# Performance work log

Hardware: AMD Instinct MI355X
Metric: run time of the kernel (lower is better)

## Reference

```python
import jax, jax.numpy as jnp
import numpy as np

B = 64
SEG = 4096
N = B * SEG
C = 512
MID = 4 * C
EPS = 1e-5


def setup_inputs() -> dict:
    key = jax.random.key(0)
    ks = jax.random.split(key, 8)
    s_in = 1.0 / np.sqrt(C)
    s_mid = 1.0 / np.sqrt(MID)
    return {
        "x2": jax.random.normal(ks[0], (N, C), dtype=jnp.float32),
        "npoint": jnp.full((B,), SEG, dtype=jnp.int64) if jax.config.jax_enable_x64 else jnp.full((B,), SEG, dtype=jnp.int32),
        "W1a": jax.random.normal(ks[1], (C, MID), dtype=jnp.float32) * s_in,
        "g1a": jnp.ones((MID,), dtype=jnp.float32),
        "b1a": jnp.zeros((MID,), dtype=jnp.float32),
        "W2a": jax.random.normal(ks[2], (MID, C), dtype=jnp.float32) * s_mid,
        "W1b": jax.random.normal(ks[3], (C, MID), dtype=jnp.float32) * s_in,
        "g1b": jnp.ones((MID,), dtype=jnp.float32),
        "b1b": jnp.zeros((MID,), dtype=jnp.float32),
        "W2b": jax.random.normal(ks[4], (MID, C), dtype=jnp.float32) * s_mid,
    }


def _bn(h, g, b):
    # training-mode BatchNorm1d over the segment (batch) axis
    m = jnp.mean(h, axis=0)
    v = jnp.var(h, axis=0)
    return (h - m) * jax.lax.rsqrt(v + EPS) * g + b


def reference(x2, npoint, W1a, g1a, b1a, W2a, W1b, g1b, b1b, W2b):
    n = x2.shape[0]
    b = npoint.shape[0]
    # segment id for every point: seg[j] = i  iff  cumsum(npoint)[i-1] <= j < cumsum(npoint)[i]
    cum = jnp.cumsum(npoint)
    seg = jnp.searchsorted(cum, jnp.arange(n), side="right")  # [N]
    counts = npoint.astype(x2.dtype)  # [B]
    # per-segment mean  [B, C]
    mean_f = jax.ops.segment_sum(x2, seg, num_segments=b) / counts[:, None]
    # fc branch: Linear -> BN -> ReLU -> Linear -> ReLU
    ha = jax.nn.relu(_bn(mean_f @ W1a, g1a, b1a))
    out_mean = jax.nn.relu(ha @ W2a)  # [B, C]
    # fc1 branch + sigmoid
    hb = jax.nn.relu(_bn(mean_f @ W1b, g1b, b1b))
    out_w = jax.nn.sigmoid(jax.nn.relu(hb @ W2b))  # [B, C]
    # broadcast per-segment stats back to points and combine
    return out_w[seg] * x2 * 0.5 + x2 * 0.75 + out_mean[seg]
```

## Files before the change

kernel.cpp:

```cpp
#include <hip/hip_runtime.h>
#include <hip/hip_bf16.h>
#include <math.h>

#define NB    64
#define CD    512
#define CV    128
#define MIDD  2048
#define RS    32
#define EPSV  1e-5f

__device__ __forceinline__ float wave_sum64(float x) {
    #pragma unroll
    for (int o = 32; o; o >>= 1) x += __shfl_xor(x, o, 64);
    return x;
}

__global__ __launch_bounds__(128) void k_partial(const float* __restrict__ x2,
                          const int* __restrict__ npoint,
                          float* __restrict__ P) {
    int bx = blockIdx.x;
    int b  = bx >> 5;
    int rs = bx & (RS - 1);
    int start = 0;
    for (int i = 0; i < b; ++i) start += npoint[i];
    int len   = npoint[b];
    int chunk = (len + RS - 1) / RS;
    int r0 = rs * chunk;
    int r1 = min(r0 + chunk, len);
    int t = threadIdx.x;
    const float4* xv = (const float4*)x2;
    float4 acc = make_float4(0.f, 0.f, 0.f, 0.f);
    #pragma unroll 8
    for (int r = r0; r < r1; ++r) {
        float4 v = xv[(size_t)(start + r) * CV + t];
        acc.x += v.x; acc.y += v.y; acc.z += v.z; acc.w += v.w;
    }
    ((float4*)P)[(size_t)bx * CV + t] = acc;
}

__global__ __launch_bounds__(128) void k_mean(const float* __restrict__ P,
                       const int* __restrict__ npoint,
                       float* __restrict__ mean_t,
                       int* __restrict__ cum) {
    int b = blockIdx.x;
    int t = threadIdx.x;
    const float4* Pv = (const float4*)P;
    float4 acc = make_float4(0.f, 0.f, 0.f, 0.f);
    #pragma unroll
    for (int rs = 0; rs < RS; ++rs) {
        float4 v = Pv[((size_t)(b * RS + rs)) * CV + t];
        acc.x += v.x; acc.y += v.y; acc.z += v.z; acc.w += v.w;
    }
    float inv = 1.0f / (float)npoint[b];
    int c = 4 * t;
    mean_t[(size_t)(c + 0) * NB + b] = acc.x * inv;
    mean_t[(size_t)(c + 1) * NB + b] = acc.y * inv;
    mean_t[(size_t)(c + 2) * NB + b] = acc.z * inv;
    mean_t[(size_t)(c + 3) * NB + b] = acc.w * inv;
    if (t == 0) {
        int s = 0;
        for (int i = 0; i <= b; ++i) s += npoint[i];
        cum[b] = s;
    }
}

__global__ __launch_bounds__(512) void k_fc1(const float* __restrict__ mean_t,
                                             const float* __restrict__ W1a,
                                             const float* __restrict__ g1a,
                                             const float* __restrict__ b1a,
                                             const float* __restrict__ W1b,
                                             const float* __restrict__ g1b,
                                             const float* __restrict__ b1b,
                                             float* __restrict__ h_t) {
    __shared__ float red[8][64][9];
    int bx = blockIdx.x;
    int branch = bx >> 8;
    int cg = bx & 255;
    int c0 = cg * 8;
    const float* W1 = branch ? W1b : W1a;
    const float* g  = branch ? g1b : g1a;
    const float* bb = branch ? b1b : b1a;
    int t = threadIdx.x;
    int lane = t & 63;
    int w = t >> 6;
    float acc[8];
    #pragma unroll
    for (int i = 0; i < 8; ++i) acc[i] = 0.f;
    int k0 = w * 64;
    for (int k = k0; k < k0 + 64; ++k) {
        float mval = mean_t[(size_t)k * NB + lane];
        const float4* wr = (const float4*)(W1 + (size_t)k * MIDD + c0);
        float4 w0 = wr[0], w1 = wr[1];
        acc[0] += mval * w0.x; acc[1] += mval * w0.y;
        acc[2] += mval * w0.z; acc[3] += mval * w0.w;
        acc[4] += mval * w1.x; acc[5] += mval * w1.y;
        acc[6] += mval * w1.z; acc[7] += mval * w1.w;
    }
    #pragma unroll
    for (int i = 0; i < 8; ++i) red[w][lane][i] = acc[i];
    __syncthreads();
    float v = red[0][lane][w];
    #pragma unroll
    for (int ww = 1; ww < 8; ++ww) v += red[ww][lane][w];
    float s = wave_sum64(v);
    float m = s * (1.0f / 64.0f);
    float d = v - m;
    float q = wave_sum64(d * d);
    float var = q * (1.0f / 64.0f);
    float val = fmaxf(d * rsqrtf(var + EPSV) * g[c0 + w] + bb[c0 + w], 0.0f);
    h_t[((size_t)branch * MIDD + c0 + w) * NB + lane] = val;
}

__global__ __launch_bounds__(512) void k_fc2(const float* __restrict__ h_t,
                                             const float* __restrict__ W2a,
                                             const float* __restrict__ W2b,
                                             float* __restrict__ out_mean,
                                             float* __restrict__ out_w) {
    __shared__ float red[8][64][9];
    int bx = blockIdx.x;
    int branch = bx >> 6;
    int cg = bx & 63;
    int c0 = cg * 8;
    const float* W2 = branch ? W2b : W2a;
    int t = threadIdx.x;
    int lane = t & 63;
    int w = t >> 6;
    float acc[8];
    #pragma unroll
    for (int i = 0; i < 8; ++i) acc[i] = 0.f;
    int k0 = w * 256;
    for (int k = k0; k < k0 + 256; ++k) {
        float hv = h_t[((size_t)branch * MIDD + k) * NB + lane];
        const float4* wr = (const float4*)(W2 + (size_t)k * CD + c0);
        float4 w0 = wr[0], w1 = wr[1];
        acc[0] += hv * w0.x; acc[1] += hv * w0.y;
        acc[2] += hv * w0.z; acc[3] += hv * w0.w;
        acc[4] += hv * w1.x; acc[5] += hv * w1.y;
        acc[6] += hv * w1.z; acc[7] += hv * w1.w;
    }
    #pragma unroll
    for (int i = 0; i < 8; ++i) red[w][lane][i] = acc[i];
    __syncthreads();
    float v = red[0][lane][w];
    #pragma unroll
    for (int ww = 1; ww < 8; ++ww) v += red[ww][lane][w];
    float r = fmaxf(v, 0.0f);
    if (branch)
        out_w[(size_t)lane * CD + c0 + w] = 1.0f / (1.0f + expf(-r));
    else
        out_mean[(size_t)lane * CD + c0 + w] = r;
}

__global__ __launch_bounds__(256) void k_final(const float* __restrict__ x2,
                        const int* __restrict__ cum,
                        const float* __restrict__ out_mean,
                        const float* __restrict__ out_w,
                        float* __restrict__ out) {
    int t = threadIdx.x;
    int lane = t & 63;
    int w = t >> 6;
    size_t base = (size_t)blockIdx.x << 10;
    int base_row = blockIdx.x << 3;
    int row = base_row + 2 * lane + (w >> 1);
    int lo = 0, hi = NB - 1;
    while (lo < hi) {
        int mid = (lo + hi) >> 1;
        if (cum[mid] > row) hi = mid; else lo = mid + 1;
    }
    const float4* xv = (const float4*)x2;
    const float4* wv = (const float4*)out_w;
    const float4* mv = (const float4*)out_mean;
    float4* ov = (float4*)out;
    int colv = t & 127;
    float4 x0 = xv[base + t];
    float4 x1 = xv[base + 256 + t];
    float4 x2v = xv[base + 512 + t];
    float4 x3 = xv[base + 768 + t];
    float4 xs[4] = {x0, x1, x2v, x3};
    #pragma unroll
    for (int k = 0; k < 4; ++k) {
        int seg = __shfl(lo, k, 64);
        float4 x = xs[k];
        float4 ww = wv[(size_t)seg * CV + colv];
        float4 mm = mv[(size_t)seg * CV + colv];
        float4 o;
        o.x = x.x * (0.5f * ww.x + 0.75f) + mm.x;
        o.y = x.y * (0.5f * ww.y + 0.75f) + mm.y;
        o.z = x.z * (0.5f * ww.z + 0.75f) + mm.z;
        o.w = x.w * (0.5f * ww.w + 0.75f) + mm.w;
        ov[base + ((size_t)k << 8) + t] = o;
    }
}

extern "C" void kernel_launch(void* const* d_in, const int* in_sizes, int n_in,
                              void* d_out, int out_size, void* d_ws, size_t ws_size,
                              hipStream_t stream) {
    const float* x2  = (const float*)d_in[0];
    const int*   npt = (const int*)d_in[1];
    const float* W1a = (const float*)d_in[2];
    const float* g1a = (const float*)d_in[3];
    const float* b1a = (const float*)d_in[4];
    const float* W2a = (const float*)d_in[5];
    const float* W1b = (const float*)d_in[6];
    const float* g1b = (const float*)d_in[7];
    const float* b1b = (const float*)d_in[8];
    const float* W2b = (const float*)d_in[9];
    float* out = (float*)d_out;

    const int N   = in_sizes[0] / CD;
    const int NC4 = (N * CD) / 4;

    float* P      = out;
    float* mean_t = out + (size_t)NB * RS * CD;
    float* h_t    = mean_t + (size_t)NB * CD;
    int*   cum      = (int*)d_ws;
    float* out_mean = (float*)d_ws + 64;
    float* out_w    = out_mean + (size_t)NB * CD;

    k_partial<<<NB * RS, 128, 0, stream>>>(x2, npt, P);
    k_mean<<<NB, 128, 0, stream>>>(P, npt, mean_t, cum);
    k_fc1<<<2 * (MIDD / 8), 512, 0, stream>>>(mean_t, W1a, g1a, b1a, W1b, g1b, b1b, h_t);
    k_fc2<<<2 * (CD / 8), 512, 0, stream>>>(h_t, W2a, W2b, out_mean, out_w);
    k_final<<<NC4 / 1024, 256, 0, stream>>>(x2, cum, out_mean, out_w, out);
}
```

Measured before the change: 374.3 us.

## Widen final kernel with nontemporal IO, reverse block order, uniform-segment fast path

The final broadcast kernel now handles 16 rows per block instead of 8. It loads x2 and stores the output with nontemporal hints, and it walks the blocks in reverse order so it can reuse x2 data left in cache by the reduction pass. A per-block check catches the common case where every row falls in one segment, so the segment weights are loaded once. The partial-sum split also doubles from 32 to 64 chunks to give the reduction more parallelism. Risks: the reversed order may not line up with the cache state, and the extra P buffer writes and the larger k_mean reduction add traffic.

```diff
diff --git a/kernel.cpp b/kernel.cpp
--- a/kernel.cpp
+++ b/kernel.cpp
@@ -6,20 +6,32 @@
 #define CD    512
 #define CV    128
 #define MIDD  2048
-#define RS    32
+#define RS    64
 #define EPSV  1e-5f
+#define FPT   8
+
+typedef float fx4 __attribute__((ext_vector_type(4)));
 
 __device__ __forceinline__ float wave_sum64(float x) {
     #pragma unroll
     for (int o = 32; o; o >>= 1) x += __shfl_xor(x, o, 64);
     return x;
+}
+
+__device__ __forceinline__ int seg_search(const int* __restrict__ cum, int row) {
+    int lo = 0, hi = NB - 1;
+    while (lo < hi) {
+        int mid = (lo + hi) >> 1;
+        if (cum[mid] > row) hi = mid; else lo = mid + 1;
+    }
+    return lo;
 }
 
 __global__ __launch_bounds__(128) void k_partial(const float* __restrict__ x2,
                           const int* __restrict__ npoint,
                           float* __restrict__ P) {
     int bx = blockIdx.x;
-    int b  = bx >> 5;
+    int b  = bx >> 6;
     int rs = bx & (RS - 1);
     int start = 0;
     for (int i = 0; i < b; ++i) start += npoint[i];
@@ -46,7 +58,7 @@
     int t = threadIdx.x;
     const float4* Pv = (const float4*)P;
     float4 acc = make_float4(0.f, 0.f, 0.f, 0.f);
-    #pragma unroll
+    #pragma unroll 8
     for (int rs = 0; rs < RS; ++rs) {
         float4 v = Pv[((size_t)(b * RS + rs)) * CV + t];
         acc.x += v.x; acc.y += v.y; acc.z += v.z; acc.w += v.w;
@@ -157,38 +169,42 @@
                         const float* __restrict__ out_w,
                         float* __restrict__ out) {
     int t = threadIdx.x;
-    int lane = t & 63;
-    int w = t >> 6;
-    size_t base = (size_t)blockIdx.x << 10;
-    int base_row = blockIdx.x << 3;
-    int row = base_row + 2 * lane + (w >> 1);
-    int lo = 0, hi = NB - 1;
-    while (lo < hi) {
-        int mid = (lo + hi) >> 1;
-        if (cum[mid] > row) hi = mid; else lo = mid + 1;
-    }
-    const float4* xv = (const float4*)x2;
-    const float4* wv = (const float4*)out_w;
-    const float4* mv = (const float4*)out_mean;
-    float4* ov = (float4*)out;
+    int bx = (int)gridDim.x - 1 - (int)blockIdx.x;
+    size_t base = (size_t)bx << 11;
+    int base_row = bx << 4;
+    const fx4* xv = (const fx4*)x2;
+    const fx4* wv = (const fx4*)out_w;
+    const fx4* mv = (const fx4*)out_mean;
+    fx4* ov = (fx4*)out;
+
+    fx4 xs[FPT];
+    #pragma unroll
+    for (int k = 0; k < FPT; ++k)
+        xs[k] = __builtin_nontemporal_load(&xv[base + ((size_t)k << 8) + t]);
+
+    int seg_lo = seg_search(cum, base_row);
+    int seg_hi = seg_search(cum, base_row + 15);
     int colv = t & 127;
-    float4 x0 = xv[base + t];
-    float4 x1 = xv[base + 256 + t];
-    float4 x2v = xv[base + 512 + t];
-    float4 x3 = xv[base + 768 + t];
-    float4 xs[4] = {x0, x1, x2v, x3};
-    #pragma unroll
-    for (int k = 0; k < 4; ++k) {
-        int seg = __shfl(lo, k, 64);
-        float4 x = xs[k];
-        float4 ww = wv[(size_t)seg * CV + colv];
-        float4 mm = mv[(size_t)seg * CV + colv];
-        float4 o;
-        o.x = x.x * (0.5f * ww.x + 0.75f) + mm.x;
-        o.y = x.y * (0.5f * ww.y + 0.75f) + mm.y;
-        o.z = x.z * (0.5f * ww.z + 0.75f) + mm.z;
-        o.w = x.w * (0.5f * ww.w + 0.75f) + mm.w;
-        ov[base + ((size_t)k << 8) + t] = o;
+
+    if (seg_lo == seg_hi) {
+        fx4 ww = wv[(size_t)seg_lo * CV + colv];
+        fx4 mm = mv[(size_t)seg_lo * CV + colv];
+        fx4 a = ww * 0.5f + 0.75f;
+        #pragma unroll
+        for (int k = 0; k < FPT; ++k) {
+            fx4 o = xs[k] * a + mm;
+            __builtin_nontemporal_store(o, &ov[base + ((size_t)k << 8) + t]);
+        }
+    } else {
+        #pragma unroll
+        for (int k = 0; k < FPT; ++k) {
+            int row = base_row + ((k * 256 + t) >> 7);
+            int seg = seg_search(cum, row);
+            fx4 ww = wv[(size_t)seg * CV + colv];
+            fx4 mm = mv[(size_t)seg * CV + colv];
+            fx4 o = xs[k] * (ww * 0.5f + 0.75f) + mm;
+            __builtin_nontemporal_store(o, &ov[base + ((size_t)k << 8) + t]);
+        }
     }
 }
 
@@ -221,5 +237,5 @@
     k_mean<<<NB, 128, 0, stream>>>(P, npt, mean_t, cum);
     k_fc1<<<2 * (MIDD / 8), 512, 0, stream>>>(mean_t, W1a, g1a, b1a, W1b, g1b, b1b, h_t);
     k_fc2<<<2 * (CD / 8), 512, 0, stream>>>(h_t, W2a, W2b, out_mean, out_w);
-    k_final<<<NC4 / 1024, 256, 0, stream>>>(x2, cum, out_mean, out_w, out);
-}
+    k_final<<<NC4 / (256 * FPT), 256, 0, stream>>>(x2, cum, out_mean, out_w, out);
+}
```

New measurement: 363.6 us. 1.03x faster.
